# Kernel optimization log

Measured on AMD Instinct MI355X. Metric: run time of the kernel, lower is better.

Reference implementation:

```python
import jax, jax.numpy as jnp
import numpy as np

EPS = 1e-5

def conv2d(x, w, b, stride, pad):
    # x: [B,C,H,W], w: [O,I,kh,kw] (NCHW / OIHW)
    y = jax.lax.conv_general_dilated(
        x, w, window_strides=(stride, stride),
        padding=[(pad, pad), (pad, pad)],
        dimension_numbers=('NCHW', 'OIHW', 'NCHW'))
    return y + b[None, :, None, None]

def bn(x, g, b, m, v):
    # inference-mode BatchNorm2d
    inv = g * jax.lax.rsqrt(v + EPS)
    return x * inv[None, :, None, None] + (b - m * inv)[None, :, None, None]

def setup_inputs() -> dict:
    key = jax.random.key(0)
    ks = jax.random.split(key, 16)
    B, Cin, Cout, H, W = 8, 512, 256, 48, 48
    r = 4
    init = lambda k, shape, fan: (jax.random.normal(k, shape, jnp.float32) / np.sqrt(fan)).astype(jnp.float32)
    d = {}
    d['x'] = jax.random.normal(ks[0], (B, Cin, H, W), jnp.float32)
    # pre_conv (3x3, Cin->Cout) + BN
    d['w_pre'] = init(ks[1], (Cout, Cin, 3, 3), Cin * 9)
    d['b_pre'] = jnp.zeros((Cout,), jnp.float32)
    d['bn1_g'] = jnp.ones((Cout,), jnp.float32)
    d['bn1_b'] = jnp.zeros((Cout,), jnp.float32)
    d['bn1_m'] = 0.1 * jax.random.normal(ks[2], (Cout,), jnp.float32)
    d['bn1_v'] = jax.random.uniform(ks[3], (Cout,), jnp.float32, 0.5, 1.5)
    # 1x1 query/key (Cout -> Cout//r) and value (Cout -> Cout)
    d['w_q'] = init(ks[4], (Cout // r, Cout, 1, 1), Cout)
    d['b_q'] = jnp.zeros((Cout // r,), jnp.float32)
    d['w_k'] = init(ks[5], (Cout // r, Cout, 1, 1), Cout)
    d['b_k'] = jnp.zeros((Cout // r,), jnp.float32)
    d['w_v'] = init(ks[6], (Cout, Cout, 1, 1), Cout)
    d['b_v'] = jnp.zeros((Cout,), jnp.float32)
    # final_conv (3x3, Cout->Cout) + BN
    d['w_f'] = init(ks[7], (Cout, Cout, 3, 3), Cout * 9)
    d['b_f'] = jnp.zeros((Cout,), jnp.float32)
    d['bn2_g'] = jnp.ones((Cout,), jnp.float32)
    d['bn2_b'] = jnp.zeros((Cout,), jnp.float32)
    d['bn2_m'] = 0.1 * jax.random.normal(ks[8], (Cout,), jnp.float32)
    d['bn2_v'] = jax.random.uniform(ks[9], (Cout,), jnp.float32, 0.5, 1.5)
    # gamma (torch init is zeros; use 0.1 so attention path contributes)
    d['gamma'] = jnp.full((1,), 0.1, jnp.float32)
    return d

def reference(x, w_pre, b_pre, bn1_g, bn1_b, bn1_m, bn1_v,
              w_q, b_q, w_k, b_k, w_v, b_v,
              w_f, b_f, bn2_g, bn2_b, bn2_m, bn2_v, gamma):
    x = jax.nn.relu(bn(conv2d(x, w_pre, b_pre, 1, 1), bn1_g, bn1_b, bn1_m, bn1_v))
    B, C, H, W = x.shape
    N = H * W
    q = conv2d(x, w_q, b_q, 1, 0).reshape(B, -1, N)   # [B, C/r, N]
    k = conv2d(x, w_k, b_k, 1, 0).reshape(B, -1, N)   # [B, C/r, N]
    energy = jnp.einsum('bci,bcj->bij', q, k)          # [B, N, N], unscaled
    attn = jax.nn.softmax(energy, axis=-1)
    v = conv2d(x, w_v, b_v, 1, 0).reshape(B, C, N)     # [B, C, N]
    out = jnp.einsum('bij,bcj->bci', attn, v).reshape(B, C, H, W)
    out_feat = gamma[0] * out + x
    out_feat = jax.nn.relu(bn(conv2d(out_feat, w_f, b_f, 1, 1), bn2_g, bn2_b, bn2_m, bn2_v))
    return out_feat
```

## Files before the change

kernel.cpp:

```cpp
#include <hip/hip_runtime.h>


typedef __attribute__((ext_vector_type(8))) short short8;
typedef __attribute__((ext_vector_type(4))) float f32x4;

#define MFMA16(A,B,C) __builtin_amdgcn_mfma_f32_16x16x32_bf16((A),(B),(C),0,0,0)

#define NB   8
#define CIN  512
#define CC   256
#define NPIX 2304
#define HWD  48
#define EPSF 1e-5f
#define NSPLIT 4
#define JT_PER 18
#define LOG2E 1.4426950408889634f
#define FIXM 32.0f

typedef unsigned short u16;
typedef unsigned int   u32;

__device__ __forceinline__ u16 f2bf(float f) {
  union { float f; u32 u; } v; v.f = f;
  u32 r = v.u + 0x7FFFu + ((v.u >> 16) & 1u);
  return (u16)(r >> 16);
}
__device__ __forceinline__ float bf2f(u16 h) {
  union { u32 u; float f; } v; v.u = ((u32)h) << 16; return v.f;
}
__device__ __forceinline__ float exp2fast(float x) {
  float r; asm("v_exp_f32 %0, %1" : "=v"(r) : "v"(x)); return r;
}
__device__ __forceinline__ u32 cvtpk(float lo, float hi) {
  u32 r; asm("v_cvt_pk_bf16_f32 %0, %1, %2" : "=v"(r) : "v"(lo), "v"(hi)); return r;
}

__global__ void fold_bn(const float* __restrict__ b_pre,
                        const float* __restrict__ g1, const float* __restrict__ bb1,
                        const float* __restrict__ m1, const float* __restrict__ v1,
                        const float* __restrict__ b_f,
                        const float* __restrict__ g2, const float* __restrict__ bb2,
                        const float* __restrict__ m2, const float* __restrict__ v2,
                        float* __restrict__ fold) {
  int c = threadIdx.x;
  if (c < CC) {
    float inv1 = g1[c] / sqrtf(v1[c] + EPSF);
    fold[c]        = inv1;
    fold[CC + c]   = (b_pre[c] - m1[c]) * inv1 + bb1[c];
    float inv2 = g2[c] / sqrtf(v2[c] + EPSF);
    fold[2*CC + c] = inv2;
    fold[3*CC + c] = (b_f[c] - m2[c]) * inv2 + bb2[c];
  }
}

__global__ void halo_zero(u16* __restrict__ xTh, u16* __restrict__ ofTh) {
  int p = blockIdx.x;
  int b = blockIdx.y;
  int hr, wc;
  if (p < 50)       { hr = 0;       wc = p; }
  else if (p < 100) { hr = 49;      wc = p - 50; }
  else if (p < 148) { hr = p - 99;  wc = 0; }
  else              { hr = p - 147; wc = 49; }
  int t = threadIdx.x;
  *(u32*)&xTh[(((size_t)b * 50 + hr) * 50 + wc) * CIN + t * 2] = 0;
  if (t < 128)
    *(u32*)&ofTh[(((size_t)b * 50 + hr) * 50 + wc) * CC + t * 2] = 0;
}

__launch_bounds__(256)
__global__ void transpose_x(const float* __restrict__ x, u16* __restrict__ xTh) {
  __shared__ u16 t[32][33];
  int tid = threadIdx.x;
  int n0 = blockIdx.x * 32, c0 = blockIdx.y * 32, b = blockIdx.z;
#pragma unroll
  for (int it = 0; it < 4; ++it) {
    int cc = (tid >> 5) + it * 8;
    int nn = tid & 31;
    t[nn][cc] = f2bf(x[((size_t)(b * CIN + c0 + cc)) * NPIX + n0 + nn]);
  }
  __syncthreads();
#pragma unroll
  for (int it = 0; it < 2; ++it) {
    int nn = (tid >> 4) + it * 16;
    int cc2 = (tid & 15) * 2;
    u32 o = (u32)t[nn][cc2] | ((u32)t[nn][cc2 + 1] << 16);
    int n = n0 + nn;
    int h = n / HWD, w = n % HWD;
    *(u32*)&xTh[(((size_t)b * 50 + h + 1) * 50 + (w + 1)) * CIN + c0 + cc2] = o;
  }
}

__launch_bounds__(256)
__global__ void conv_w(const float* __restrict__ wpre, const float* __restrict__ wf,
                       const float* __restrict__ wq, const float* __restrict__ wk,
                       const float* __restrict__ wvw,
                       u16* __restrict__ wbpre, u16* __restrict__ wbf,
                       u16* __restrict__ wqb, u16* __restrict__ wkb,
                       u16* __restrict__ wvb) {
  int idx = blockIdx.x * 256 + threadIdx.x;
  if (idx < 1179648) {
    int tap = idx / 131072, rem = idx % 131072;
    int co = rem >> 9, ci = rem & 511;
    wbpre[idx] = f2bf(wpre[((size_t)co * CIN + ci) * 9 + tap]);
  } else if (idx < 1769472) {
    int j = idx - 1179648;
    int tap = j / 65536, rem = j % 65536;
    int co = rem >> 8, ci = rem & 255;
    wbf[j] = f2bf(wf[((size_t)co * CC + ci) * 9 + tap]);
  } else if (idx < 1785856) {
    int j = idx - 1769472; wqb[j] = f2bf(wq[j] * LOG2E);
  } else if (idx < 1802240) {
    int j = idx - 1785856; wkb[j] = f2bf(wk[j]);
  } else if (idx < 1867776) {
    int j = idx - 1802240; wvb[j] = f2bf(wvw[j]);
  }
}

template<int CINT, bool TOUT>
__launch_bounds__(256)
__global__ void conv_mfma(const u16* __restrict__ inTh, const u16* __restrict__ wb,
                          const float* __restrict__ scale, const float* __restrict__ shift,
                          u16* __restrict__ outB, float* __restrict__ outF) {
  __shared__ u16 xs[200 * 40];
  __shared__ u16 wsl[576 * 40];
  int tid = threadIdx.x;
  int lane = tid & 63, wv = tid >> 6;
  int l15 = lane & 15, g = lane >> 4;
  int hb = blockIdx.x, cob = blockIdx.y * 64, b = blockIdx.z;

  f32x4 z4 = {0.f, 0.f, 0.f, 0.f};
  f32x4 acc[2][3];
#pragma unroll
  for (int r = 0; r < 2; ++r)
#pragma unroll
    for (int t = 0; t < 3; ++t) acc[r][t] = z4;

  const u16* xb = inTh + ((size_t)b * 50 + 2 * hb) * 50 * CINT;

#pragma unroll 1
  for (int ci0 = 0; ci0 < CINT; ci0 += 32) {
    __syncthreads();
#pragma unroll
    for (int s4 = 0; s4 < 4; ++s4) {
      int s = tid + s4 * 256;
      if (s < 800) {
        int r = s >> 2, q = s & 3;
        int rr = r / 50, cc = r % 50;
        *(uint4*)&xs[r * 40 + q * 8] =
            *(const uint4*)&xb[((size_t)(rr * 50 + cc)) * CINT + ci0 + q * 8];
      }
    }
#pragma unroll
    for (int it = 0; it < 9; ++it) {
      int slot = tid + it * 256;
      int row = slot >> 2, q4 = slot & 3;
      *((uint4*)&wsl[row * 40] + q4) =
          *(const uint4*)&wb[((size_t)((row >> 6) * 256 + cob + (row & 63))) * CINT + ci0 + q4 * 8];
    }
    __syncthreads();
#pragma unroll
    for (int kh = 0; kh < 3; ++kh) {
#pragma unroll
      for (int kw = 0; kw < 3; ++kw) {
        int tap = kh * 3 + kw;
        short8 wf = *(const short8*)&wsl[((tap * 64) + wv * 16 + l15) * 40 + g * 8];
#pragma unroll
        for (int r = 0; r < 2; ++r)
#pragma unroll
          for (int t = 0; t < 3; ++t) {
            short8 xf = *(const short8*)
                &xs[((r + kh) * 50 + t * 16 + l15 + kw) * 40 + g * 8];
            if constexpr (TOUT) acc[r][t] = MFMA16(xf, wf, acc[r][t]);
            else                acc[r][t] = MFMA16(wf, xf, acc[r][t]);
          }
      }
    }
  }

  if constexpr (TOUT) {
    int co = cob + wv * 16 + l15;
    float sc = scale[co], sh = shift[co];
#pragma unroll
    for (int r = 0; r < 2; ++r)
#pragma unroll
      for (int t = 0; t < 3; ++t)
#pragma unroll
        for (int rr = 0; rr < 4; ++rr) {
          int px = (2 * hb + r) * HWD + t * 16 + 4 * g + rr;
          float v = fmaxf(fmaf(acc[r][t][rr], sc, sh), 0.f);
          outB[((size_t)b * NPIX + px) * CC + co] = f2bf(v);
        }
  } else {
#pragma unroll
    for (int rr = 0; rr < 4; ++rr) {
      int co = cob + wv * 16 + 4 * g + rr;
      float sc = scale[co], sh = shift[co];
#pragma unroll
      for (int r = 0; r < 2; ++r)
#pragma unroll
        for (int t = 0; t < 3; ++t) {
          int px = (2 * hb + r) * HWD + t * 16 + l15;
          float v = fmaxf(fmaf(acc[r][t][rr], sc, sh), 0.f);
          outF[((size_t)b * CC + co) * NPIX + px] = v;
        }
    }
  }
}

__launch_bounds__(256)
__global__ void qkv_mfma(const u16* __restrict__ x1T,
                         const u16* __restrict__ wqb, const u16* __restrict__ wkb,
                         const u16* __restrict__ wvb,
                         const float* __restrict__ b_q, const float* __restrict__ b_k,
                         const float* __restrict__ b_v,
                         u16* __restrict__ qb, u16* __restrict__ kb,
                         u16* __restrict__ vb) {
  __shared__ u16 xt[32 * 264];
  __shared__ u16 wt[64 * 264];
  int tid = threadIdx.x;
  int lane = tid & 63, wv = tid >> 6;
  int l15 = lane & 15, g = lane >> 4;
  int n0 = blockIdx.x * 32, y = blockIdx.y, b = blockIdx.z;
  const u16* w; const float* bias; int mb = 0; float bsc = 1.f;
  if (y == 0)      { w = wqb; bias = b_q; bsc = LOG2E; }
  else if (y == 1) { w = wkb; bias = b_k; }
  else             { w = wvb; bias = b_v; mb = (y - 2) * 64; }
  {
    int row = tid >> 3, s = (tid & 7) * 32;
    const uint4* src = (const uint4*)&x1T[((size_t)b * NPIX + n0 + row) * CC + s];
    uint4* dst = (uint4*)&xt[row * 264 + s];
    dst[0] = src[0]; dst[1] = src[1]; dst[2] = src[2]; dst[3] = src[3];
  }
  {
    int row = tid >> 2, s = (tid & 3) * 64;
    const uint4* src = (const uint4*)&w[((size_t)(mb + row)) * CC + s];
    uint4* dst = (uint4*)&wt[row * 264 + s];
#pragma unroll
    for (int u = 0; u < 8; ++u) dst[u] = src[u];
  }
  __syncthreads();
  f32x4 z4 = {0.f, 0.f, 0.f, 0.f};
  f32x4 acc[2] = {z4, z4};
  if (y <= 1) {
#pragma unroll
    for (int cc = 0; cc < 8; ++cc) {
      short8 wf = *(const short8*)&wt[(wv * 16 + l15) * 264 + cc * 32 + g * 8];
#pragma unroll
      for (int nt = 0; nt < 2; ++nt) {
        short8 xf = *(const short8*)&xt[(nt * 16 + l15) * 264 + cc * 32 + g * 8];
        acc[nt] = MFMA16(xf, wf, acc[nt]);
      }
    }
    u16* outp = (y == 0) ? qb : kb;
    int m = wv * 16 + l15;
    float bi = bias[m] * bsc;
#pragma unroll
    for (int nt = 0; nt < 2; ++nt)
#pragma unroll
      for (int r = 0; r < 4; ++r) {
        int n = n0 + nt * 16 + 4 * g + r;
        outp[((size_t)b * NPIX + n) * 64 + m] = f2bf(acc[nt][r] + bi);
      }
  } else {
#pragma unroll
    for (int cc = 0; cc < 8; ++cc) {
      short8 wf = *(const short8*)&wt[(wv * 16 + l15) * 264 + cc * 32 + g * 8];
#pragma unroll
      for (int nt = 0; nt < 2; ++nt) {
        short8 xf = *(const short8*)&xt[(nt * 16 + l15) * 264 + cc * 32 + g * 8];
        acc[nt] = MFMA16(wf, xf, acc[nt]);
      }
    }
    int mrow = mb + wv * 16 + 4 * g;
#pragma unroll
    for (int r = 0; r < 4; ++r) {
      float bi = bias[mrow + r];
#pragma unroll
      for (int nt = 0; nt < 2; ++nt) {
        int n = n0 + nt * 16 + l15;
        vb[((size_t)b * CC + mrow + r) * NPIX + n] = f2bf(acc[nt][r] + bi);
      }
    }
  }
}

__launch_bounds__(256)
__global__ void flash_mfma(const u16* __restrict__ qbp, const u16* __restrict__ kbp,
                           const u16* __restrict__ vbp,
                           u16* __restrict__ opart, float* __restrict__ dpart) {
  __shared__ u16 pb[4][32 * 40];
  int tid = threadIdx.x;
  int lane = tid & 63, wv = tid >> 6;
  int l15 = lane & 15, g = lane >> 4;
  int i0 = blockIdx.x * 32, sp = blockIdx.y, b = blockIdx.z;
  u16* pbw = pb[wv];

  short8 qf[2][2];
#pragma unroll
  for (int it = 0; it < 2; ++it)
#pragma unroll
    for (int cc = 0; cc < 2; ++cc)
      qf[it][cc] = *(const short8*)
          &qbp[((size_t)b * NPIX + i0 + it * 16 + l15) * 64 + cc * 32 + g * 8];

  f32x4 z4 = {0.f, 0.f, 0.f, 0.f};
  f32x4 acc[4][2];
#pragma unroll
  for (int ct = 0; ct < 4; ++ct) { acc[ct][0] = z4; acc[ct][1] = z4; }
  float d_l[2] = {0.f, 0.f};

  const u16* kb0 = kbp + (size_t)b * NPIX * 64;
  const u16* vb0 = vbp + ((size_t)b * CC + wv * 64) * NPIX;
  int jbase = sp * JT_PER * 32;

  short8 kf[2][2];
#pragma unroll
  for (int jh = 0; jh < 2; ++jh)
#pragma unroll
    for (int cc = 0; cc < 2; ++cc)
      kf[jh][cc] = *(const short8*)
          &kb0[(size_t)(jbase + jh * 16 + l15) * 64 + cc * 32 + g * 8];

#pragma unroll 1
  for (int jt = 0; jt < JT_PER; ++jt) {
    int j0 = jbase + jt * 32;
    short8 vf[4];
#pragma unroll
    for (int ct = 0; ct < 4; ++ct)
      vf[ct] = *(const short8*)&vb0[(size_t)(ct * 16 + l15) * NPIX + j0 + g * 8];

    f32x4 s[2][2];
#pragma unroll
    for (int jh = 0; jh < 2; ++jh)
#pragma unroll
      for (int it = 0; it < 2; ++it) {
        s[jh][it] = MFMA16(kf[jh][0], qf[it][0], z4);
        s[jh][it] = MFMA16(kf[jh][1], qf[it][1], s[jh][it]);
      }

    int j0n = (jt + 1 < JT_PER) ? j0 + 32 : jbase;
    short8 kn[2][2];
#pragma unroll
    for (int jh = 0; jh < 2; ++jh)
#pragma unroll
      for (int cc = 0; cc < 2; ++cc)
        kn[jh][cc] = *(const short8*)
            &kb0[(size_t)(j0n + jh * 16 + l15) * 64 + cc * 32 + g * 8];

#pragma unroll
    for (int it = 0; it < 2; ++it) {
      float p[8];
      float sum = 0.f;
#pragma unroll
      for (int jh = 0; jh < 2; ++jh)
#pragma unroll
        for (int r = 0; r < 4; ++r) {
          float pv = exp2fast(s[jh][it][r] - FIXM);
          p[jh * 4 + r] = pv; sum += pv;
        }
      d_l[it] += sum;
#pragma unroll
      for (int jh = 0; jh < 2; ++jh) {
        uint2 pk;
        pk.x = cvtpk(p[jh * 4 + 0], p[jh * 4 + 1]);
        pk.y = cvtpk(p[jh * 4 + 2], p[jh * 4 + 3]);
        *(uint2*)&pbw[(it * 16 + l15) * 40 + jh * 16 + 4 * g] = pk;
      }
    }
    short8 pf0 = *(const short8*)&pbw[l15 * 40 + g * 8];
    short8 pf1 = *(const short8*)&pbw[(16 + l15) * 40 + g * 8];
#pragma unroll
    for (int ct = 0; ct < 4; ++ct) {
      acc[ct][0] = MFMA16(vf[ct], pf0, acc[ct][0]);
      acc[ct][1] = MFMA16(vf[ct], pf1, acc[ct][1]);
    }
#pragma unroll
    for (int jh = 0; jh < 2; ++jh)
#pragma unroll
      for (int cc = 0; cc < 2; ++cc) kf[jh][cc] = kn[jh][cc];
  }

#pragma unroll
  for (int it = 0; it < 2; ++it) {
    float d = d_l[it];
    d += __shfl_xor(d, 16);
    d += __shfl_xor(d, 32);
    d_l[it] = d;
  }
  size_t orow = (size_t)(sp * NB + b) * NPIX;
#pragma unroll
  for (int it = 0; it < 2; ++it) {
    int i = i0 + it * 16 + l15;
#pragma unroll
    for (int ct = 0; ct < 4; ++ct)
#pragma unroll
      for (int r = 0; r < 4; ++r) {
        int c = wv * 64 + ct * 16 + 4 * g + r;
        opart[(orow + i) * CC + c] = f2bf(acc[ct][it][r]);
      }
    if (wv == 0 && g == 0) dpart[orow + i] = d_l[it];
  }
}

__launch_bounds__(256)
__global__ void flash_combine(const u16* __restrict__ opart,
                              const float* __restrict__ dpart,
                              const u16* __restrict__ x1T,
                              const float* __restrict__ gamma,
                              u16* __restrict__ ofTh) {
  int t = threadIdx.x;
  int i = blockIdx.x * 8 + (t >> 5);
  int b = blockIdx.y;
  int c8 = (t & 31) * 8;
  float D = 0.f;
#pragma unroll
  for (int s = 0; s < NSPLIT; ++s) D += dpart[(size_t)(s * NB + b) * NPIX + i];
  float o[8];
#pragma unroll
  for (int e = 0; e < 8; ++e) o[e] = 0.f;
#pragma unroll
  for (int s = 0; s < NSPLIT; ++s) {
    short8 v = *(const short8*)&opart[((size_t)(s * NB + b) * NPIX + i) * CC + c8];
#pragma unroll
    for (int e = 0; e < 8; ++e) o[e] += bf2f((u16)v[e]);
  }
  float gmD = gamma[0] / D;
  size_t xidx = ((size_t)b * NPIX + i) * CC + c8;
  short8 x1v = *(const short8*)&x1T[xidx];
  short8 outv;
#pragma unroll
  for (int e = 0; e < 8; ++e)
    outv[e] = (short)f2bf(o[e] * gmD + bf2f((u16)x1v[e]));
  int h = i / HWD, w = i % HWD;
  *(short8*)&ofTh[(((size_t)b * 50 + h + 1) * 50 + (w + 1)) * CC + c8] = outv;
}

extern "C" void kernel_launch(void* const* d_in, const int* in_sizes, int n_in,
                              void* d_out, int out_size, void* d_ws, size_t ws_size,
                              hipStream_t stream) {
  (void)in_sizes; (void)n_in; (void)out_size; (void)ws_size;
  const float* x     = (const float*)d_in[0];
  const float* w_pre = (const float*)d_in[1];
  const float* b_pre = (const float*)d_in[2];
  const float* bn1_g = (const float*)d_in[3];
  const float* bn1_b = (const float*)d_in[4];
  const float* bn1_m = (const float*)d_in[5];
  const float* bn1_v = (const float*)d_in[6];
  const float* w_q   = (const float*)d_in[7];
  const float* b_q   = (const float*)d_in[8];
  const float* w_k   = (const float*)d_in[9];
  const float* b_k   = (const float*)d_in[10];
  const float* w_v   = (const float*)d_in[11];
  const float* b_v   = (const float*)d_in[12];
  const float* w_f   = (const float*)d_in[13];
  const float* b_f   = (const float*)d_in[14];
  const float* bn2_g = (const float*)d_in[15];
  const float* bn2_b = (const float*)d_in[16];
  const float* bn2_m = (const float*)d_in[17];
  const float* bn2_v = (const float*)d_in[18];
  const float* gamma = (const float*)d_in[19];
  float* out = (float*)d_out;

  u16* wsu   = (u16*)d_ws;
  u16* xTh   = wsu;
  u16* x1T   = wsu + 10240000;
  u16* qb    = wsu + 14958592;
  u16* kb    = wsu + 16138240;
  u16* vb    = wsu + 17317888;
  u16* ofTh  = wsu + 22036480;
  u16* wbpre = wsu + 27156480;
  u16* wbf   = wsu + 28336128;
  u16* wqb   = wsu + 28925952;
  u16* wkb   = wsu + 28942336;
  u16* wvb   = wsu + 28958720;
  float* fold = (float*)(wsu + 29024256);
  u16* opart = wsu + 29026304;
  float* dpart = (float*)(wsu + 47900672);

  fold_bn<<<1, 256, 0, stream>>>(b_pre, bn1_g, bn1_b, bn1_m, bn1_v,
                                 b_f, bn2_g, bn2_b, bn2_m, bn2_v, fold);
  halo_zero<<<dim3(196, 8), 256, 0, stream>>>(xTh, ofTh);
  transpose_x<<<dim3(72, 16, 8), 256, 0, stream>>>(x, xTh);
  conv_w<<<7296, 256, 0, stream>>>(w_pre, w_f, w_q, w_k, w_v,
                                   wbpre, wbf, wqb, wkb, wvb);
  conv_mfma<512, true><<<dim3(24, 4, 8), 256, 0, stream>>>(
      xTh, wbpre, fold, fold + 256, x1T, nullptr);
  qkv_mfma<<<dim3(72, 6, 8), 256, 0, stream>>>(
      x1T, wqb, wkb, wvb, b_q, b_k, b_v, qb, kb, vb);
  flash_mfma<<<dim3(72, NSPLIT, 8), 256, 0, stream>>>(qb, kb, vb, opart, dpart);
  flash_combine<<<dim3(NPIX / 8, 8), 256, 0, stream>>>(opart, dpart, x1T, gamma, ofTh);
  conv_mfma<256, false><<<dim3(24, 4, 8), 256, 0, stream>>>(
      ofTh, wbf, fold + 512, fold + 768, nullptr, out);
}
```

Baseline: 433.4 us.

## Split QK^T and softmax work across waves, share P tile via LDS

Before, each of the four waves recomputed the full 32x32 score tile (8 MFMAs plus 16 exps per lane) for its own channel slice, duplicating that work four times. Now each wave computes one 16x16 quadrant, writes its bf16 probabilities into a shared double-buffered LDS tile, and a workgroup barrier precedes the PV MFMAs. Row sums are reduced across waves through LDS at the end. This removes redundant MFMA, exp and K-load work, at the cost of one block-wide barrier per j-tile.

After: 397.1 us. -8.4%, faster.

```diff
diff --git a/kernel.cpp b/kernel.cpp
--- a/kernel.cpp
+++ b/kernel.cpp
@@ -288,38 +288,35 @@
 __global__ void flash_mfma(const u16* __restrict__ qbp, const u16* __restrict__ kbp,
                            const u16* __restrict__ vbp,
                            u16* __restrict__ opart, float* __restrict__ dpart) {
-  __shared__ u16 pb[4][32 * 40];
+  __shared__ u16 pb[2][32 * 40];
+  __shared__ float dls[4][16];
   int tid = threadIdx.x;
   int lane = tid & 63, wv = tid >> 6;
   int l15 = lane & 15, g = lane >> 4;
+  int qit = wv >> 1, qjh = wv & 1;
   int i0 = blockIdx.x * 32, sp = blockIdx.y, b = blockIdx.z;
-  u16* pbw = pb[wv];
-
-  short8 qf[2][2];
-#pragma unroll
-  for (int it = 0; it < 2; ++it)
-#pragma unroll
-    for (int cc = 0; cc < 2; ++cc)
-      qf[it][cc] = *(const short8*)
-          &qbp[((size_t)b * NPIX + i0 + it * 16 + l15) * 64 + cc * 32 + g * 8];
+
+  short8 qf[2];
+#pragma unroll
+  for (int cc = 0; cc < 2; ++cc)
+    qf[cc] = *(const short8*)
+        &qbp[((size_t)b * NPIX + i0 + qit * 16 + l15) * 64 + cc * 32 + g * 8];
 
   f32x4 z4 = {0.f, 0.f, 0.f, 0.f};
   f32x4 acc[4][2];
 #pragma unroll
   for (int ct = 0; ct < 4; ++ct) { acc[ct][0] = z4; acc[ct][1] = z4; }
-  float d_l[2] = {0.f, 0.f};
+  float d_l = 0.f;
 
   const u16* kb0 = kbp + (size_t)b * NPIX * 64;
   const u16* vb0 = vbp + ((size_t)b * CC + wv * 64) * NPIX;
   int jbase = sp * JT_PER * 32;
 
-  short8 kf[2][2];
-#pragma unroll
-  for (int jh = 0; jh < 2; ++jh)
-#pragma unroll
-    for (int cc = 0; cc < 2; ++cc)
-      kf[jh][cc] = *(const short8*)
-          &kb0[(size_t)(jbase + jh * 16 + l15) * 64 + cc * 32 + g * 8];
+  short8 kf[2];
+#pragma unroll
+  for (int cc = 0; cc < 2; ++cc)
+    kf[cc] = *(const short8*)
+        &kb0[(size_t)(jbase + qjh * 16 + l15) * 64 + cc * 32 + g * 8];
 
 #pragma unroll 1
   for (int jt = 0; jt < JT_PER; ++jt) {
@@ -329,65 +326,50 @@
     for (int ct = 0; ct < 4; ++ct)
       vf[ct] = *(const short8*)&vb0[(size_t)(ct * 16 + l15) * NPIX + j0 + g * 8];
 
-    f32x4 s[2][2];
-#pragma unroll
-    for (int jh = 0; jh < 2; ++jh)
-#pragma unroll
-      for (int it = 0; it < 2; ++it) {
-        s[jh][it] = MFMA16(kf[jh][0], qf[it][0], z4);
-        s[jh][it] = MFMA16(kf[jh][1], qf[it][1], s[jh][it]);
-      }
+    f32x4 s = MFMA16(kf[0], qf[0], z4);
+    s = MFMA16(kf[1], qf[1], s);
 
     int j0n = (jt + 1 < JT_PER) ? j0 + 32 : jbase;
-    short8 kn[2][2];
-#pragma unroll
-    for (int jh = 0; jh < 2; ++jh)
-#pragma unroll
-      for (int cc = 0; cc < 2; ++cc)
-        kn[jh][cc] = *(const short8*)
-            &kb0[(size_t)(j0n + jh * 16 + l15) * 64 + cc * 32 + g * 8];
-
-#pragma unroll
-    for (int it = 0; it < 2; ++it) {
-      float p[8];
-      float sum = 0.f;
-#pragma unroll
-      for (int jh = 0; jh < 2; ++jh)
-#pragma unroll
-        for (int r = 0; r < 4; ++r) {
-          float pv = exp2fast(s[jh][it][r] - FIXM);
-          p[jh * 4 + r] = pv; sum += pv;
-        }
-      d_l[it] += sum;
-#pragma unroll
-      for (int jh = 0; jh < 2; ++jh) {
-        uint2 pk;
-        pk.x = cvtpk(p[jh * 4 + 0], p[jh * 4 + 1]);
-        pk.y = cvtpk(p[jh * 4 + 2], p[jh * 4 + 3]);
-        *(uint2*)&pbw[(it * 16 + l15) * 40 + jh * 16 + 4 * g] = pk;
-      }
-    }
-    short8 pf0 = *(const short8*)&pbw[l15 * 40 + g * 8];
-    short8 pf1 = *(const short8*)&pbw[(16 + l15) * 40 + g * 8];
+    short8 kn[2];
+#pragma unroll
+    for (int cc = 0; cc < 2; ++cc)
+      kn[cc] = *(const short8*)
+          &kb0[(size_t)(j0n + qjh * 16 + l15) * 64 + cc * 32 + g * 8];
+
+    float p[4];
+#pragma unroll
+    for (int r = 0; r < 4; ++r) p[r] = exp2fast(s[r] - FIXM);
+    d_l += (p[0] + p[1]) + (p[2] + p[3]);
+    uint2 pk;
+    pk.x = cvtpk(p[0], p[1]);
+    pk.y = cvtpk(p[2], p[3]);
+    int buf = jt & 1;
+    *(uint2*)&pb[buf][(qit * 16 + l15) * 40 + qjh * 16 + 4 * g] = pk;
+
+    asm volatile("s_waitcnt lgkmcnt(0)" ::: "memory");
+    __builtin_amdgcn_s_barrier();
+    __builtin_amdgcn_sched_barrier(0);
+
+    short8 pf0 = *(const short8*)&pb[buf][l15 * 40 + g * 8];
+    short8 pf1 = *(const short8*)&pb[buf][(16 + l15) * 40 + g * 8];
 #pragma unroll
     for (int ct = 0; ct < 4; ++ct) {
       acc[ct][0] = MFMA16(vf[ct], pf0, acc[ct][0]);
       acc[ct][1] = MFMA16(vf[ct], pf1, acc[ct][1]);
     }
-#pragma unroll
-    for (int jh = 0; jh < 2; ++jh)
-#pragma unroll
-      for (int cc = 0; cc < 2; ++cc) kf[jh][cc] = kn[jh][cc];
-  }
-
-#pragma unroll
-  for (int it = 0; it < 2; ++it) {
-    float d = d_l[it];
-    d += __shfl_xor(d, 16);
-    d += __shfl_xor(d, 32);
-    d_l[it] = d;
-  }
+    kf[0] = kn[0]; kf[1] = kn[1];
+  }
+
+  d_l += __shfl_xor(d_l, 16);
+  d_l += __shfl_xor(d_l, 32);
+  if (g == 0) dls[wv][l15] = d_l;
+  __syncthreads();
+
   size_t orow = (size_t)(sp * NB + b) * NPIX;
+  if (wv == 0 && lane < 32) {
+    int it = lane >> 4, l = lane & 15;
+    dpart[orow + i0 + lane] = dls[2 * it][l] + dls[2 * it + 1][l];
+  }
 #pragma unroll
   for (int it = 0; it < 2; ++it) {
     int i = i0 + it * 16 + l15;
@@ -398,7 +380,6 @@
         int c = wv * 64 + ct * 16 + 4 * g + r;
         opart[(orow + i) * CC + c] = f2bf(acc[ct][it][r]);
       }
-    if (wv == 0 && g == 0) dpart[orow + i] = d_l[it];
   }
 }
 
```
